# Optimization experiments

Hardware: AMD Instinct MI355X
Metric: run time of the kernel (lower is better)

Reference implementation:

```python
import jax, jax.numpy as jnp
import numpy as np

# multi-scale pyramid (low2high: lowest resolution first), d_model etc. from module defaults
SHAPES = ((8, 8), (16, 16), (32, 32), (64, 64))
D, HEADS, DH, PTS, NLV, NLAYERS, DFF = 256, 8, 32, 4, 4, 6, 1024
L_TOTAL = sum(h * w for h, w in SHAPES)  # 5440
B = 4


def _ref_points():
    # normalized (x, y) pixel centers per level, concatenated -> [L_TOTAL, 2]
    pts = []
    for (H, W) in SHAPES:
        ry = (jnp.arange(H, dtype=jnp.float32) + 0.5) / H
        rx = (jnp.arange(W, dtype=jnp.float32) + 0.5) / W
        gy, gx = jnp.meshgrid(ry, rx, indexing='ij')
        pts.append(jnp.stack([gx.ravel(), gy.ravel()], -1))
    return jnp.concatenate(pts, 0)


def _lev_ids():
    return jnp.concatenate([jnp.full((h * w,), l, dtype=jnp.int32)
                            for l, (h, w) in enumerate(SHAPES)])


def _layer_norm(x, g, b):
    m = jnp.mean(x, -1, keepdims=True)
    v = jnp.mean((x - m) ** 2, -1, keepdims=True)
    return g * (x - m) * jax.lax.rsqrt(v + 1e-5) + b


def _ms_deform_attn(q, src, ref, w_off, b_off, w_attn, b_attn, w_val, b_val, w_out, b_out):
    Bq, L, _ = q.shape
    v = (src @ w_val + b_val).reshape(Bq, L, HEADS, DH)
    off = (q @ w_off + b_off).reshape(Bq, L, HEADS, NLV, PTS, 2)
    aw = jax.nn.softmax((q @ w_attn + b_attn).reshape(Bq, L, HEADS, NLV * PTS), -1)
    aw = aw.reshape(Bq, L, HEADS, NLV, PTS)
    # offset normalizer is (W, H) per level
    norm = jnp.array([[w, h] for (h, w) in SHAPES], dtype=q.dtype)
    loc = ref[None, :, None, None, None, :] + off / norm[None, None, None, :, None, :]
    out = jnp.zeros((Bq, L, HEADS, DH), q.dtype)
    start = 0
    for l, (H_, W_) in enumerate(SHAPES):
        vl = v[:, start:start + H_ * W_].transpose(0, 2, 1, 3)  # [B, heads, HW, dh]
        # grid_sample(align_corners=False): pixel coord = loc * size - 0.5
        x = loc[:, :, :, l, :, 0] * W_ - 0.5  # [B, L, heads, P]
        y = loc[:, :, :, l, :, 1] * H_ - 0.5
        x0 = jnp.floor(x).astype(jnp.int32)
        y0 = jnp.floor(y).astype(jnp.int32)
        fx = x - x0
        fy = y - y0

        def corner(ix, iy, w):
            inb = ((ix >= 0) & (ix < W_) & (iy >= 0) & (iy < H_)).astype(q.dtype)
            idx = jnp.clip(iy, 0, H_ - 1) * W_ + jnp.clip(ix, 0, W_ - 1)
            idx = idx.transpose(0, 2, 1, 3).reshape(Bq, HEADS, L * PTS, 1)
            g = jnp.take_along_axis(vl, idx, axis=2)  # [B, heads, L*P, dh]
            wt = (w * inb).transpose(0, 2, 1, 3).reshape(Bq, HEADS, L * PTS, 1)
            return g * wt

        samp = (corner(x0, y0, (1 - fx) * (1 - fy))
                + corner(x0 + 1, y0, fx * (1 - fy))
                + corner(x0, y0 + 1, (1 - fx) * fy)
                + corner(x0 + 1, y0 + 1, fx * fy))
        samp = samp.reshape(Bq, HEADS, L, PTS, DH)
        out = out + jnp.einsum('blhp,bhlpd->blhd', aw[:, :, :, l, :], samp)
        start += H_ * W_
    return out.reshape(Bq, L, D) @ w_out + b_out


def setup_inputs() -> dict:
    key = jax.random.key(0)
    ks = jax.random.split(key, 16)
    s = 0.02
    inp = {
        'src': jax.random.normal(ks[0], (B, L_TOTAL, D), jnp.float32),
        'pos': jax.random.normal(ks[1], (B, L_TOTAL, D), jnp.float32),
        'level_embed': jax.random.normal(ks[2], (NLV, D), jnp.float32),
        'w_off': jax.random.normal(ks[3], (NLAYERS, D, HEADS * NLV * PTS * 2), jnp.float32) * s,
        'b_off': jnp.zeros((NLAYERS, HEADS * NLV * PTS * 2), jnp.float32),
        'w_attn': jax.random.normal(ks[4], (NLAYERS, D, HEADS * NLV * PTS), jnp.float32) * s,
        'b_attn': jnp.zeros((NLAYERS, HEADS * NLV * PTS), jnp.float32),
        'w_val': jax.random.normal(ks[5], (NLAYERS, D, D), jnp.float32) * s,
        'b_val': jnp.zeros((NLAYERS, D), jnp.float32),
        'w_out': jax.random.normal(ks[6], (NLAYERS, D, D), jnp.float32) * s,
        'b_out': jnp.zeros((NLAYERS, D), jnp.float32),
        'ln1_g': jnp.ones((NLAYERS, D), jnp.float32),
        'ln1_b': jnp.zeros((NLAYERS, D), jnp.float32),
        'w_ff1': jax.random.normal(ks[7], (NLAYERS, D, DFF), jnp.float32) * s,
        'b_ff1': jnp.zeros((NLAYERS, DFF), jnp.float32),
        'w_ff2': jax.random.normal(ks[8], (NLAYERS, DFF, D), jnp.float32) * s,
        'b_ff2': jnp.zeros((NLAYERS, D), jnp.float32),
        'ln2_g': jnp.ones((NLAYERS, D), jnp.float32),
        'ln2_b': jnp.zeros((NLAYERS, D), jnp.float32),
    }
    return inp


def reference(src, pos, level_embed, w_off, b_off, w_attn, b_attn, w_val, b_val,
              w_out, b_out, ln1_g, ln1_b, w_ff1, b_ff1, w_ff2, b_ff2, ln2_g, ln2_b):
    # lvl_pos_embed = pos + level_embed[level-of-token] (masks all False -> valid_ratios == 1)
    lvl_pos = pos + level_embed[_lev_ids()]
    ref = _ref_points().astype(src.dtype)
    x = src
    for i in range(NLAYERS):
        q = x + lvl_pos
        x2 = _ms_deform_attn(q, x, ref, w_off[i], b_off[i], w_attn[i], b_attn[i],
                             w_val[i], b_val[i], w_out[i], b_out[i])
        x = _layer_norm(x + x2, ln1_g[i], ln1_b[i])
        ff = jax.nn.relu(x @ w_ff1[i] + b_ff1[i]) @ w_ff2[i] + b_ff2[i]
        x = _layer_norm(x + ff, ln2_g[i], ln2_b[i])
    return x
```

## Files before the change

kernel.cpp:

```cpp
#include <hip/hip_runtime.h>

#define LTOT 5440
#define NTOK 21760

typedef float  f32x4  __attribute__((ext_vector_type(4)));
typedef short  short8 __attribute__((ext_vector_type(8)));

__device__ __forceinline__ unsigned short f2bf(float f) {
  unsigned int u = __float_as_uint(f);
  u += 0x7FFF + ((u >> 16) & 1);
  return (unsigned short)(u >> 16);
}

__global__ void wconv(const float* __restrict__ w_off, const float* __restrict__ w_attn,
                      const float* __restrict__ w_val, const float* __restrict__ w_out,
                      const float* __restrict__ w_ff1, const float* __restrict__ w_ff2,
                      unsigned short* __restrict__ dst) {
  int tid = blockIdx.x * 256 + threadIdx.x;
  const int PER = 753664;
  if (tid >= 6 * PER) return;
  int layer = tid / PER;
  int rem = tid - layer * PER;
  int base, K, N;
  const float* src;
  if (rem < 65536)       { base = 0;      K = 256;  N = 256;  src = w_off; }
  else if (rem < 98304)  { base = 65536;  K = 256;  N = 128;  src = w_attn; }
  else if (rem < 163840) { base = 98304;  K = 256;  N = 256;  src = w_val; }
  else if (rem < 229376) { base = 163840; K = 256;  N = 256;  src = w_out; }
  else if (rem < 491520) { base = 229376; K = 256;  N = 1024; src = w_ff1; }
  else                   { base = 491520; K = 1024; N = 256;  src = w_ff2; }
  int local = rem - base;
  int n = local / K, k = local - n * K;
  dst[tid] = f2bf(src[(size_t)layer * K * N + (size_t)k * N + n]);
}

__global__ void prep(const float* __restrict__ src, float* __restrict__ x,
                     unsigned short* __restrict__ xb) {
  int i = blockIdx.x * 256 + threadIdx.x;
  float4 s = ((const float4*)src)[i];
  ((float4*)x)[i] = s;
  ushort4 o;
  o.x = f2bf(s.x); o.y = f2bf(s.y); o.z = f2bf(s.z); o.w = f2bf(s.w);
  ((ushort4*)xb)[i] = o;
}

__global__ void qadd(const float* __restrict__ x, const float* __restrict__ pos,
                     const float* __restrict__ lev_emb, unsigned short* __restrict__ qb) {
  int i = blockIdx.x * 256 + threadIdx.x;
  int d4 = i & 63;
  int tok = (i >> 6) % LTOT;
  int lev = (tok < 64) ? 0 : (tok < 320) ? 1 : (tok < 1344) ? 2 : 3;
  float4 xv = ((const float4*)x)[i];
  float4 pv = ((const float4*)pos)[i];
  float4 lv = ((const float4*)lev_emb)[lev * 64 + d4];
  ushort4 o;
  o.x = f2bf(xv.x + pv.x + lv.x);
  o.y = f2bf(xv.y + pv.y + lv.y);
  o.z = f2bf(xv.z + pv.z + lv.z);
  o.w = f2bf(xv.w + pv.w + lv.w);
  ((ushort4*)qb)[i] = o;
}

template<bool RELU, bool OBF16>
__global__ __launch_bounds__(256) void gemm_tn(
    const unsigned short* __restrict__ A, const unsigned short* __restrict__ Wt,
    const float* __restrict__ bias, void* __restrict__ Cout,
    int M, int N, int K) {
  __shared__ __align__(16) unsigned short a_lds[128 * 64];
  __shared__ __align__(16) unsigned short b_lds[128 * 64];
  int m0 = blockIdx.x * 128;
  int n0 = blockIdx.y * 128;
  int t = threadIdx.x;
  int w = t >> 6, l = t & 63;
  int wr = (w >> 1) * 64, wc = (w & 1) * 64;
  int lr = l & 15, lk = (l >> 4) * 8;

  f32x4 acc[4][4] = {};

  for (int k0 = 0; k0 < K; k0 += 64) {
#pragma unroll
    for (int i = 0; i < 4; ++i) {
      int c = i * 256 + t;
      int row = c >> 3, off8 = (c & 7) * 8;
      const unsigned short* gp = A + (size_t)(m0 + row) * K + k0 + off8;
      __builtin_amdgcn_global_load_lds(
          (const __attribute__((address_space(1))) void*)gp,
          (__attribute__((address_space(3))) void*)(a_lds + c * 8), 16, 0, 0);
    }
#pragma unroll
    for (int i = 0; i < 4; ++i) {
      int c = i * 256 + t;
      int row = c >> 3, off8 = (c & 7) * 8;
      const unsigned short* gp = Wt + (size_t)(n0 + row) * K + k0 + off8;
      __builtin_amdgcn_global_load_lds(
          (const __attribute__((address_space(1))) void*)gp,
          (__attribute__((address_space(3))) void*)(b_lds + c * 8), 16, 0, 0);
    }
    __syncthreads();
#pragma unroll
    for (int kk = 0; kk < 64; kk += 32) {
      short8 af[4], bfr[4];
#pragma unroll
      for (int m = 0; m < 4; ++m)
        af[m] = *(const short8*)(a_lds + (wr + m * 16 + lr) * 64 + kk + lk);
#pragma unroll
      for (int n = 0; n < 4; ++n)
        bfr[n] = *(const short8*)(b_lds + (wc + n * 16 + lr) * 64 + kk + lk);
#pragma unroll
      for (int m = 0; m < 4; ++m)
#pragma unroll
        for (int n = 0; n < 4; ++n)
          acc[m][n] = __builtin_amdgcn_mfma_f32_16x16x32_bf16(af[m], bfr[n], acc[m][n], 0, 0, 0);
    }
    __syncthreads();
  }

  int rb = (l >> 4) * 4;
#pragma unroll
  for (int n = 0; n < 4; ++n) {
    int col = n0 + wc + n * 16 + lr;
    float bv = bias[col];
#pragma unroll
    for (int m = 0; m < 4; ++m) {
#pragma unroll
      for (int r = 0; r < 4; ++r) {
        int row = m0 + wr + m * 16 + rb + r;
        float v = acc[m][n][r] + bv;
        if (RELU) v = fmaxf(v, 0.0f);
        if (OBF16) ((unsigned short*)Cout)[(size_t)row * N + col] = f2bf(v);
        else       ((float*)Cout)[(size_t)row * N + col] = v;
      }
    }
  }
}

__global__ void softmax16(float* __restrict__ a) {
  int row = blockIdx.x * 256 + threadIdx.x;
  float4* p = ((float4*)a) + (size_t)row * 4;
  float4 v0 = p[0], v1 = p[1], v2 = p[2], v3 = p[3];
  float vv[16] = {v0.x, v0.y, v0.z, v0.w, v1.x, v1.y, v1.z, v1.w,
                  v2.x, v2.y, v2.z, v2.w, v3.x, v3.y, v3.z, v3.w};
  float m = vv[0];
#pragma unroll
  for (int i = 1; i < 16; ++i) m = fmaxf(m, vv[i]);
  float s = 0.0f;
#pragma unroll
  for (int i = 0; i < 16; ++i) { vv[i] = __expf(vv[i] - m); s += vv[i]; }
  float inv = 1.0f / s;
#pragma unroll
  for (int i = 0; i < 16; ++i) vv[i] *= inv;
  p[0] = make_float4(vv[0], vv[1], vv[2], vv[3]);
  p[1] = make_float4(vv[4], vv[5], vv[6], vv[7]);
  p[2] = make_float4(vv[8], vv[9], vv[10], vv[11]);
  p[3] = make_float4(vv[12], vv[13], vv[14], vv[15]);
}

__global__ __launch_bounds__(256) void ms_sample(
    const float* __restrict__ offp, const float* __restrict__ attnp,
    const float* __restrict__ v, unsigned short* __restrict__ samp) {
  __shared__ int   sIdx[128 * 4];
  __shared__ float sWt[128 * 4];
  int bl = blockIdx.x;
  int t = threadIdx.x;
  int l = bl % LTOT;
  int bbase = (bl - l) * 256;
  if (t < 128) {
    int lev = (t >> 2) & 3;
    int lev_q = (l < 64) ? 0 : (l < 320) ? 1 : (l < 1344) ? 2 : 3;
    int start_q = (lev_q == 0) ? 0 : (lev_q == 1) ? 64 : (lev_q == 2) ? 320 : 1344;
    int shq = lev_q + 3;
    int r = l - start_q;
    int Wq = 1 << shq;
    int iy = r >> shq, ix = r & (Wq - 1);
    float invWq = 1.0f / (float)Wq;
    float refx = ((float)ix + 0.5f) * invWq;
    float refy = ((float)iy + 0.5f) * invWq;
    int iW = 8 << lev;
    float Wl = (float)iW;
    int start_l = (lev == 0) ? 0 : (lev == 1) ? 64 : (lev == 2) ? 320 : 1344;
    float ox = offp[bl * 256 + 2 * t];
    float oy = offp[bl * 256 + 2 * t + 1];
    float aw = attnp[bl * 128 + t];
    float gx = refx * Wl + ox - 0.5f;
    float gy = refy * Wl + oy - 0.5f;
    float flx = floorf(gx), fly = floorf(gy);
    int x0 = (int)flx, y0 = (int)fly;
    float fx = gx - flx, fy = gy - fly;
#pragma unroll
    for (int c = 0; c < 4; ++c) {
      int cx = x0 + (c & 1);
      int cy = y0 + (c >> 1);
      int inb = (cx >= 0) && (cx < iW) && (cy >= 0) && (cy < iW);
      int cxc = cx < 0 ? 0 : (cx > iW - 1 ? iW - 1 : cx);
      int cyc = cy < 0 ? 0 : (cy > iW - 1 ? iW - 1 : cy);
      float wx = (c & 1) ? fx : 1.0f - fx;
      float wy = (c & 2) ? fy : 1.0f - fy;
      sIdx[t * 4 + c] = (start_l + cyc * iW + cxc) * 256;
      sWt[t * 4 + c] = inb ? aw * wx * wy : 0.0f;
    }
  }
  __syncthreads();
  int h = t >> 5;
  int sbase = h * 64;
  float acc = 0.0f;
#pragma unroll 4
  for (int s = 0; s < 16; ++s) {
#pragma unroll
    for (int c = 0; c < 4; ++c) {
      float wgt = sWt[sbase + s * 4 + c];
      int idx = sIdx[sbase + s * 4 + c];
      acc = fmaf(wgt, v[bbase + idx + t], acc);
    }
  }
  samp[(size_t)bl * 256 + t] = f2bf(acc);
}

__global__ __launch_bounds__(256) void ln_fused(
    const float* __restrict__ xin, const float* __restrict__ yin,
    const float* __restrict__ g, const float* __restrict__ bb,
    float* __restrict__ xout, unsigned short* __restrict__ xbout) {
  int row = blockIdx.x * 4 + (threadIdx.x >> 6);
  int lane = threadIdx.x & 63;
  size_t base = (size_t)row * 64 + lane;
  float4 xv = ((const float4*)xin)[base];
  float4 yv = ((const float4*)yin)[base];
  float4 tv;
  tv.x = xv.x + yv.x; tv.y = xv.y + yv.y; tv.z = xv.z + yv.z; tv.w = xv.w + yv.w;
  float s = tv.x + tv.y + tv.z + tv.w;
  float s2 = tv.x * tv.x + tv.y * tv.y + tv.z * tv.z + tv.w * tv.w;
#pragma unroll
  for (int o = 1; o < 64; o <<= 1) {
    s += __shfl_xor(s, o, 64);
    s2 += __shfl_xor(s2, o, 64);
  }
  float mean = s * (1.0f / 256.0f);
  float var = s2 * (1.0f / 256.0f) - mean * mean;
  float rstd = rsqrtf(var + 1e-5f);
  float4 gv = ((const float4*)g)[lane];
  float4 bv = ((const float4*)bb)[lane];
  float4 o;
  o.x = gv.x * (tv.x - mean) * rstd + bv.x;
  o.y = gv.y * (tv.y - mean) * rstd + bv.y;
  o.z = gv.z * (tv.z - mean) * rstd + bv.z;
  o.w = gv.w * (tv.w - mean) * rstd + bv.w;
  ((float4*)xout)[base] = o;
  ushort4 ob;
  ob.x = f2bf(o.x); ob.y = f2bf(o.y); ob.z = f2bf(o.z); ob.w = f2bf(o.w);
  ((ushort4*)xbout)[base] = ob;
}

extern "C" void kernel_launch(void* const* d_in, const int* in_sizes, int n_in,
                              void* d_out, int out_size, void* d_ws, size_t ws_size,
                              hipStream_t stream) {
  (void)in_sizes; (void)n_in; (void)out_size; (void)ws_size;
  const float* src     = (const float*)d_in[0];
  const float* pos     = (const float*)d_in[1];
  const float* lev_emb = (const float*)d_in[2];
  const float* w_off   = (const float*)d_in[3];
  const float* b_off   = (const float*)d_in[4];
  const float* w_attn  = (const float*)d_in[5];
  const float* b_attn  = (const float*)d_in[6];
  const float* w_val   = (const float*)d_in[7];
  const float* b_val   = (const float*)d_in[8];
  const float* w_out   = (const float*)d_in[9];
  const float* b_out   = (const float*)d_in[10];
  const float* ln1_g   = (const float*)d_in[11];
  const float* ln1_b   = (const float*)d_in[12];
  const float* w_ff1   = (const float*)d_in[13];
  const float* b_ff1   = (const float*)d_in[14];
  const float* w_ff2   = (const float*)d_in[15];
  const float* b_ff2   = (const float*)d_in[16];
  const float* ln2_g   = (const float*)d_in[17];
  const float* ln2_b   = (const float*)d_in[18];

  char* ws = (char*)d_ws;
  float*          x     = (float*)(ws + 0);
  float*          y     = (float*)(ws + 22282240);
  unsigned short* xb    = (unsigned short*)(ws + 44564480);
  unsigned short* qb    = (unsigned short*)(ws + 55705600);
  float*          offb  = (float*)(ws + 66846720);
  float*          attnb = (float*)(ws + 89128960);
  unsigned short* sampb = (unsigned short*)(ws + 100270080);
  unsigned short* h1    = (unsigned short*)(ws + 66846720);
  unsigned short* wT    = (unsigned short*)(ws + 111411200);

  wconv<<<17664, 256, 0, stream>>>(w_off, w_attn, w_val, w_out, w_ff1, w_ff2, wT);
  prep<<<5440, 256, 0, stream>>>(src, x, xb);

  for (int i = 0; i < 6; ++i) {
    const unsigned short* wl = wT + (size_t)i * 753664;
    qadd<<<5440, 256, 0, stream>>>(x, pos, lev_emb, qb);
    gemm_tn<false, false><<<dim3(170, 2), 256, 0, stream>>>(qb, wl + 0,      b_off + i * 256,  (void*)offb,  NTOK, 256, 256);
    gemm_tn<false, false><<<dim3(170, 1), 256, 0, stream>>>(qb, wl + 65536,  b_attn + i * 128, (void*)attnb, NTOK, 128, 256);
    gemm_tn<false, false><<<dim3(170, 2), 256, 0, stream>>>(xb, wl + 98304,  b_val + i * 256,  (void*)y,     NTOK, 256, 256);
    softmax16<<<680, 256, 0, stream>>>(attnb);
    ms_sample<<<NTOK, 256, 0, stream>>>(offb, attnb, y, sampb);
    gemm_tn<false, false><<<dim3(170, 2), 256, 0, stream>>>(sampb, wl + 163840, b_out + i * 256, (void*)y,   NTOK, 256, 256);
    ln_fused<<<5440, 256, 0, stream>>>(x, y, ln1_g + i * 256, ln1_b + i * 256, x, xb);
    gemm_tn<true,  true ><<<dim3(170, 8), 256, 0, stream>>>(xb, wl + 229376, b_ff1 + i * 1024, (void*)h1,    NTOK, 1024, 256);
    gemm_tn<false, false><<<dim3(170, 2), 256, 0, stream>>>(h1, wl + 491520, b_ff2 + i * 256,  (void*)y,     NTOK, 256, 1024);
    float* xo = (i == 5) ? (float*)d_out : x;
    ln_fused<<<5440, 256, 0, stream>>>(x, y, ln2_g + i * 256, ln2_b + i * 256, xo, xb);
  }
}
```

Before: 1.329 ms.

## Fuse offset/attention GEMMs, softmax into sampler, qadd into LN, bf16 values

Merges the offset and attention-logit projections into one N=384 GEMM with a packed bias, and moves the 16-way softmax into ms_sample using lane shuffles. The separate qadd kernel is removed by computing q in prep and in the second layernorm. The value projection is written as bf16, which halves the gather traffic in sampling, and the sampler uses two accumulators plus a block-index swizzle. This removes several launches and intermediate round trips, at the cost of bf16 rounding on the values and workspace buffer aliasing (sampb now shares space with qb).

New measurement: 1.288 ms. 3.1% less time.

```diff
diff --git a/kernel.cpp b/kernel.cpp
--- a/kernel.cpp
+++ b/kernel.cpp
@@ -10,6 +10,9 @@
   unsigned int u = __float_as_uint(f);
   u += 0x7FFF + ((u >> 16) & 1);
   return (unsigned short)(u >> 16);
+}
+__device__ __forceinline__ float bf2f(unsigned short u) {
+  return __uint_as_float(((unsigned int)u) << 16);
 }
 
 __global__ void wconv(const float* __restrict__ w_off, const float* __restrict__ w_attn,
@@ -34,31 +37,32 @@
   dst[tid] = f2bf(src[(size_t)layer * K * N + (size_t)k * N + n]);
 }
 
-__global__ void prep(const float* __restrict__ src, float* __restrict__ x,
-                     unsigned short* __restrict__ xb) {
+__global__ void bpack(const float* __restrict__ b_off, const float* __restrict__ b_attn,
+                      float* __restrict__ fb) {
+  int l = blockIdx.x, t = threadIdx.x;
+  fb[l * 384 + t] = (t < 256) ? b_off[l * 256 + t] : b_attn[l * 128 + t - 256];
+}
+
+__global__ void prep(const float* __restrict__ src, const float* __restrict__ pos,
+                     const float* __restrict__ lev_emb, float* __restrict__ x,
+                     unsigned short* __restrict__ xb, unsigned short* __restrict__ qb) {
   int i = blockIdx.x * 256 + threadIdx.x;
+  int d4 = i & 63;
+  int tok = (i >> 6) % LTOT;
+  int lev = (tok < 64) ? 0 : (tok < 320) ? 1 : (tok < 1344) ? 2 : 3;
   float4 s = ((const float4*)src)[i];
+  float4 pv = ((const float4*)pos)[i];
+  float4 lv = ((const float4*)lev_emb)[lev * 64 + d4];
   ((float4*)x)[i] = s;
   ushort4 o;
   o.x = f2bf(s.x); o.y = f2bf(s.y); o.z = f2bf(s.z); o.w = f2bf(s.w);
   ((ushort4*)xb)[i] = o;
-}
-
-__global__ void qadd(const float* __restrict__ x, const float* __restrict__ pos,
-                     const float* __restrict__ lev_emb, unsigned short* __restrict__ qb) {
-  int i = blockIdx.x * 256 + threadIdx.x;
-  int d4 = i & 63;
-  int tok = (i >> 6) % LTOT;
-  int lev = (tok < 64) ? 0 : (tok < 320) ? 1 : (tok < 1344) ? 2 : 3;
-  float4 xv = ((const float4*)x)[i];
-  float4 pv = ((const float4*)pos)[i];
-  float4 lv = ((const float4*)lev_emb)[lev * 64 + d4];
-  ushort4 o;
-  o.x = f2bf(xv.x + pv.x + lv.x);
-  o.y = f2bf(xv.y + pv.y + lv.y);
-  o.z = f2bf(xv.z + pv.z + lv.z);
-  o.w = f2bf(xv.w + pv.w + lv.w);
-  ((ushort4*)qb)[i] = o;
+  ushort4 q;
+  q.x = f2bf(s.x + pv.x + lv.x);
+  q.y = f2bf(s.y + pv.y + lv.y);
+  q.z = f2bf(s.z + pv.z + lv.z);
+  q.w = f2bf(s.w + pv.w + lv.w);
+  ((ushort4*)qb)[i] = q;
 }
 
 template<bool RELU, bool OBF16>
@@ -134,37 +138,27 @@
   }
 }
 
-__global__ void softmax16(float* __restrict__ a) {
-  int row = blockIdx.x * 256 + threadIdx.x;
-  float4* p = ((float4*)a) + (size_t)row * 4;
-  float4 v0 = p[0], v1 = p[1], v2 = p[2], v3 = p[3];
-  float vv[16] = {v0.x, v0.y, v0.z, v0.w, v1.x, v1.y, v1.z, v1.w,
-                  v2.x, v2.y, v2.z, v2.w, v3.x, v3.y, v3.z, v3.w};
-  float m = vv[0];
-#pragma unroll
-  for (int i = 1; i < 16; ++i) m = fmaxf(m, vv[i]);
-  float s = 0.0f;
-#pragma unroll
-  for (int i = 0; i < 16; ++i) { vv[i] = __expf(vv[i] - m); s += vv[i]; }
-  float inv = 1.0f / s;
-#pragma unroll
-  for (int i = 0; i < 16; ++i) vv[i] *= inv;
-  p[0] = make_float4(vv[0], vv[1], vv[2], vv[3]);
-  p[1] = make_float4(vv[4], vv[5], vv[6], vv[7]);
-  p[2] = make_float4(vv[8], vv[9], vv[10], vv[11]);
-  p[3] = make_float4(vv[12], vv[13], vv[14], vv[15]);
-}
-
 __global__ __launch_bounds__(256) void ms_sample(
-    const float* __restrict__ offp, const float* __restrict__ attnp,
-    const float* __restrict__ v, unsigned short* __restrict__ samp) {
+    const float* __restrict__ offattn, const unsigned short* __restrict__ vb,
+    unsigned short* __restrict__ samp) {
   __shared__ int   sIdx[128 * 4];
   __shared__ float sWt[128 * 4];
-  int bl = blockIdx.x;
+  int bid = blockIdx.x;
+  int bl = (bid & 7) * (NTOK / 8) + (bid >> 3);
   int t = threadIdx.x;
   int l = bl % LTOT;
   int bbase = (bl - l) * 256;
   if (t < 128) {
+    float logit = offattn[(size_t)bl * 384 + 256 + t];
+    float mx = logit;
+#pragma unroll
+    for (int o = 1; o < 16; o <<= 1) mx = fmaxf(mx, __shfl_xor(mx, o));
+    float e = __expf(logit - mx);
+    float ssum = e;
+#pragma unroll
+    for (int o = 1; o < 16; o <<= 1) ssum += __shfl_xor(ssum, o);
+    float aw = e / ssum;
+
     int lev = (t >> 2) & 3;
     int lev_q = (l < 64) ? 0 : (l < 320) ? 1 : (l < 1344) ? 2 : 3;
     int start_q = (lev_q == 0) ? 0 : (lev_q == 1) ? 64 : (lev_q == 2) ? 320 : 1344;
@@ -178,9 +172,8 @@
     int iW = 8 << lev;
     float Wl = (float)iW;
     int start_l = (lev == 0) ? 0 : (lev == 1) ? 64 : (lev == 2) ? 320 : 1344;
-    float ox = offp[bl * 256 + 2 * t];
-    float oy = offp[bl * 256 + 2 * t + 1];
-    float aw = attnp[bl * 128 + t];
+    float ox = offattn[(size_t)bl * 384 + 2 * t];
+    float oy = offattn[(size_t)bl * 384 + 2 * t + 1];
     float gx = refx * Wl + ox - 0.5f;
     float gy = refy * Wl + oy - 0.5f;
     float flx = floorf(gx), fly = floorf(gy);
@@ -202,23 +195,28 @@
   __syncthreads();
   int h = t >> 5;
   int sbase = h * 64;
-  float acc = 0.0f;
-#pragma unroll 4
+  float acc0 = 0.0f, acc1 = 0.0f;
+#pragma unroll
   for (int s = 0; s < 16; ++s) {
-#pragma unroll
-    for (int c = 0; c < 4; ++c) {
-      float wgt = sWt[sbase + s * 4 + c];
-      int idx = sIdx[sbase + s * 4 + c];
-      acc = fmaf(wgt, v[bbase + idx + t], acc);
-    }
-  }
-  samp[(size_t)bl * 256 + t] = f2bf(acc);
-}
-
+    float w0 = sWt[sbase + s * 4 + 0]; int i0 = sIdx[sbase + s * 4 + 0];
+    float w1 = sWt[sbase + s * 4 + 1]; int i1 = sIdx[sbase + s * 4 + 1];
+    float w2 = sWt[sbase + s * 4 + 2]; int i2 = sIdx[sbase + s * 4 + 2];
+    float w3 = sWt[sbase + s * 4 + 3]; int i3 = sIdx[sbase + s * 4 + 3];
+    acc0 = fmaf(w0, bf2f(vb[bbase + i0 + t]), acc0);
+    acc1 = fmaf(w1, bf2f(vb[bbase + i1 + t]), acc1);
+    acc0 = fmaf(w2, bf2f(vb[bbase + i2 + t]), acc0);
+    acc1 = fmaf(w3, bf2f(vb[bbase + i3 + t]), acc1);
+  }
+  samp[(size_t)bl * 256 + t] = f2bf(acc0 + acc1);
+}
+
+template<bool QADD>
 __global__ __launch_bounds__(256) void ln_fused(
     const float* __restrict__ xin, const float* __restrict__ yin,
     const float* __restrict__ g, const float* __restrict__ bb,
-    float* __restrict__ xout, unsigned short* __restrict__ xbout) {
+    const float* __restrict__ pos, const float* __restrict__ lev_emb,
+    float* __restrict__ xout, unsigned short* __restrict__ xbout,
+    unsigned short* __restrict__ qbout) {
   int row = blockIdx.x * 4 + (threadIdx.x >> 6);
   int lane = threadIdx.x & 63;
   size_t base = (size_t)row * 64 + lane;
@@ -247,6 +245,18 @@
   ushort4 ob;
   ob.x = f2bf(o.x); ob.y = f2bf(o.y); ob.z = f2bf(o.z); ob.w = f2bf(o.w);
   ((ushort4*)xbout)[base] = ob;
+  if (QADD) {
+    int tok = row % LTOT;
+    int lev = (tok < 64) ? 0 : (tok < 320) ? 1 : (tok < 1344) ? 2 : 3;
+    float4 pv = ((const float4*)pos)[base];
+    float4 lv = ((const float4*)lev_emb)[lev * 64 + lane];
+    ushort4 q;
+    q.x = f2bf(o.x + pv.x + lv.x);
+    q.y = f2bf(o.y + pv.y + lv.y);
+    q.z = f2bf(o.z + pv.z + lv.z);
+    q.w = f2bf(o.w + pv.w + lv.w);
+    ((ushort4*)qbout)[base] = q;
+  }
 }
 
 extern "C" void kernel_launch(void* const* d_in, const int* in_sizes, int n_in,
@@ -278,28 +288,30 @@
   float*          y     = (float*)(ws + 22282240);
   unsigned short* xb    = (unsigned short*)(ws + 44564480);
   unsigned short* qb    = (unsigned short*)(ws + 55705600);
-  float*          offb  = (float*)(ws + 66846720);
-  float*          attnb = (float*)(ws + 89128960);
-  unsigned short* sampb = (unsigned short*)(ws + 100270080);
+  unsigned short* sampb = (unsigned short*)(ws + 55705600);
+  float*          offat = (float*)(ws + 66846720);
+  unsigned short* vb    = (unsigned short*)(ws + 100270080);
   unsigned short* h1    = (unsigned short*)(ws + 66846720);
   unsigned short* wT    = (unsigned short*)(ws + 111411200);
+  float*          fb    = (float*)(ws + 120455168);
 
   wconv<<<17664, 256, 0, stream>>>(w_off, w_attn, w_val, w_out, w_ff1, w_ff2, wT);
-  prep<<<5440, 256, 0, stream>>>(src, x, xb);
+  bpack<<<6, 384, 0, stream>>>(b_off, b_attn, fb);
+  prep<<<5440, 256, 0, stream>>>(src, pos, lev_emb, x, xb, qb);
 
   for (int i = 0; i < 6; ++i) {
     const unsigned short* wl = wT + (size_t)i * 753664;
-    qadd<<<5440, 256, 0, stream>>>(x, pos, lev_emb, qb);
-    gemm_tn<false, false><<<dim3(170, 2), 256, 0, stream>>>(qb, wl + 0,      b_off + i * 256,  (void*)offb,  NTOK, 256, 256);
-    gemm_tn<false, false><<<dim3(170, 1), 256, 0, stream>>>(qb, wl + 65536,  b_attn + i * 128, (void*)attnb, NTOK, 128, 256);
-    gemm_tn<false, false><<<dim3(170, 2), 256, 0, stream>>>(xb, wl + 98304,  b_val + i * 256,  (void*)y,     NTOK, 256, 256);
-    softmax16<<<680, 256, 0, stream>>>(attnb);
-    ms_sample<<<NTOK, 256, 0, stream>>>(offb, attnb, y, sampb);
+    gemm_tn<false, false><<<dim3(170, 3), 256, 0, stream>>>(qb, wl + 0,      fb + i * 384,     (void*)offat, NTOK, 384, 256);
+    gemm_tn<false, true ><<<dim3(170, 2), 256, 0, stream>>>(xb, wl + 98304,  b_val + i * 256,  (void*)vb,    NTOK, 256, 256);
+    ms_sample<<<NTOK, 256, 0, stream>>>(offat, vb, sampb);
     gemm_tn<false, false><<<dim3(170, 2), 256, 0, stream>>>(sampb, wl + 163840, b_out + i * 256, (void*)y,   NTOK, 256, 256);
-    ln_fused<<<5440, 256, 0, stream>>>(x, y, ln1_g + i * 256, ln1_b + i * 256, x, xb);
+    ln_fused<false><<<5440, 256, 0, stream>>>(x, y, ln1_g + i * 256, ln1_b + i * 256, pos, lev_emb, x, xb, qb);
     gemm_tn<true,  true ><<<dim3(170, 8), 256, 0, stream>>>(xb, wl + 229376, b_ff1 + i * 1024, (void*)h1,    NTOK, 1024, 256);
     gemm_tn<false, false><<<dim3(170, 2), 256, 0, stream>>>(h1, wl + 491520, b_ff2 + i * 256,  (void*)y,     NTOK, 256, 1024);
     float* xo = (i == 5) ? (float*)d_out : x;
-    ln_fused<<<5440, 256, 0, stream>>>(x, y, ln2_g + i * 256, ln2_b + i * 256, xo, xb);
-  }
-}
+    if (i < 5)
+      ln_fused<true ><<<5440, 256, 0, stream>>>(x, y, ln2_g + i * 256, ln2_b + i * 256, pos, lev_emb, xo, xb, qb);
+    else
+      ln_fused<false><<<5440, 256, 0, stream>>>(x, y, ln2_g + i * 256, ln2_b + i * 256, pos, lev_emb, xo, xb, qb);
+  }
+}
```
